# Kernel optimization log

Hardware: AMD Instinct MI355X
Metric: run time of the kernel (lower is better)

The kernel has to match this reference:

```python
import jax, jax.numpy as jnp
import numpy as np
from jax import lax

DIM = 256
NUM_HEADS = 8
HEAD_DIM = DIM // NUM_HEADS
SCALE = HEAD_DIM ** -0.5
DBZ_THRESHOLD = 15.0
DILATION = 1


def setup_inputs() -> dict:
    key = jax.random.key(0)
    k_x, k_dbz, k_qkv, k_pw, k_pb = jax.random.split(key, 5)
    B, T, H, W, C = 1, 4, 32, 32, DIM
    x = jax.random.normal(k_x, (B, T, H, W, C), dtype=jnp.float32)
    dbz_values = jax.random.uniform(k_dbz, (B, T, H, W, 1), dtype=jnp.float32) * 75.0
    s = 1.0 / np.sqrt(C)
    qkv_w = jax.random.uniform(k_qkv, (3 * C, C), minval=-s, maxval=s, dtype=jnp.float32)
    proj_w = jax.random.uniform(k_pw, (C, C), minval=-s, maxval=s, dtype=jnp.float32)
    proj_b = jax.random.uniform(k_pb, (C,), minval=-s, maxval=s, dtype=jnp.float32)
    return {"x": x, "dbz_values": dbz_values, "qkv_w": qkv_w, "proj_w": proj_w, "proj_b": proj_b}


def _keep_mask(dbz_values):
    # valid precipitation tokens
    valid = dbz_values[..., 0] >= DBZ_THRESHOLD  # (B,T,H,W) bool
    B, T, H, W = valid.shape
    ksz = 2 * DILATION + 1
    vf = valid.astype(jnp.float32).reshape(B * T, H, W)
    # morphological dilation == max-pool (stride 1, zero-pad). Padding with -inf is
    # equivalent here since every window contains >=1 real pixel (value >= 0).
    dilated = lax.reduce_window(vf, -jnp.inf, lax.max,
                                (1, ksz, ksz), (1, 1, 1),
                                [(0, 0), (DILATION, DILATION), (DILATION, DILATION)])
    boundary = ((dilated > 0.5) != (vf > 0.5)).reshape(B, T, H, W)
    return valid | boundary  # hybrid keep mask


def reference(x, dbz_values, qkv_w, proj_w, proj_b):
    B, T, H, W, C = x.shape
    keep = _keep_mask(dbz_values).reshape(-1)          # (N,) over all B*T*H*W tokens
    x_flat = x.reshape(-1, C)                          # (N,C)
    N = x_flat.shape[0]

    # QKV projection (no bias)
    qkv = (x_flat @ qkv_w.T).reshape(N, 3, NUM_HEADS, HEAD_DIM)
    q = jnp.transpose(qkv[:, 0], (1, 0, 2))           # (h,N,d)
    k = jnp.transpose(qkv[:, 1], (1, 0, 2))
    v = jnp.transpose(qkv[:, 2], (1, 0, 2))

    # dense attention among kept tokens == masked attention over all tokens:
    # mask non-kept KEYS with -inf; zero out non-kept QUERY outputs afterwards.
    attn = jnp.einsum('hnd,hmd->hnm', q, k) * SCALE    # (h,N,N)
    attn = jnp.where(keep[None, None, :], attn, -jnp.inf)
    attn = jax.nn.softmax(attn, axis=-1)
    out = jnp.einsum('hnm,hmd->hnd', attn, v)          # (h,N,d)
    out = jnp.transpose(out, (1, 0, 2)).reshape(N, C)
    out = out @ proj_w.T + proj_b
    out = jnp.where(keep[:, None], out, 0.0).reshape(B, T, H, W, C)
    return out + x  # residual
```

## Files before the change

### kernel.cpp

```cpp
#include <hip/hip_runtime.h>
#include <hip/hip_bf16.h>

#define N_TOK 4096
#define NH 8
#define HD 32
#define CDIM 256
#define QKV_N 768
#define VT_STRIDE 4128
#define XB_STRIDE 272
#define SCALE_F 0.17677669529663687f
#define LOG2E   1.4426950408889634f

typedef float  f32x4  __attribute__((ext_vector_type(4)));
typedef int    i32x4  __attribute__((ext_vector_type(4)));
typedef short  s16x4  __attribute__((ext_vector_type(4)));
typedef __bf16 bf16x8 __attribute__((ext_vector_type(8)));

union FragI { i32x4 i; bf16x8 b; };
union FragH { struct { s16x4 lo, hi; } s; bf16x8 b; };

__device__ inline int pack_bf16_trunc(float a, float b) {
  return (int)__builtin_amdgcn_perm(__builtin_bit_cast(unsigned, b),
                                    __builtin_bit_cast(unsigned, a),
                                    0x07060302u);
}

#define SEG_X 1048576
#define SEG_W (SEG_X + 196608)
#define SEG_P (SEG_W + 65536)
#define SEG_M (SEG_P + 4096)
__global__ __launch_bounds__(256) void fused_prep(const float* __restrict__ x,
                                                  const float* __restrict__ qkv_w,
                                                  const float* __restrict__ proj_w,
                                                  const float* __restrict__ dbz,
                                                  __bf16* __restrict__ xb,
                                                  __bf16* __restrict__ wqkvb,
                                                  __bf16* __restrict__ wprojb,
                                                  float* __restrict__ bias,
                                                  int* __restrict__ keepi) {
  int gid = blockIdx.x * 256 + threadIdx.x;
  if (gid < SEG_X) {
    xb[(gid >> 8) * XB_STRIDE + (gid & 255)] = (__bf16)x[gid];
  } else if (gid < SEG_W) {
    int i = gid - SEG_X;
    float s = ((i >> 8) < 256) ? (SCALE_F * LOG2E) : 1.0f;
    wqkvb[(i >> 8) * XB_STRIDE + (i & 255)] = (__bf16)(qkv_w[i] * s);
  } else if (gid < SEG_P) {
    int i = gid - SEG_W;
    wprojb[(i >> 8) * XB_STRIDE + (i & 255)] = (__bf16)proj_w[i];
  } else if (gid < SEG_M) {
    int n = gid - SEG_P;
    int t = n >> 10, rc = n & 1023, r = rc >> 5, c = rc & 31;
    bool keep = false;
    #pragma unroll
    for (int dr = -1; dr <= 1; dr++)
      #pragma unroll
      for (int dc = -1; dc <= 1; dc++) {
        int rr = r + dr, cc = c + dc;
        if (rr >= 0 && rr < 32 && cc >= 0 && cc < 32)
          keep = keep || (dbz[t * 1024 + rr * 32 + cc] >= 15.0f);
      }
    bias[n]  = keep ? 0.0f : -30000.0f;
    keepi[n] = keep ? 1 : 0;
  }
}

__global__ __launch_bounds__(256) void qkv_gemm(const __bf16* __restrict__ xb,
                                                const __bf16* __restrict__ wb,
                                                __bf16* __restrict__ qb,
                                                __bf16* __restrict__ kb,
                                                __bf16* __restrict__ vt) {
  int wave = threadIdx.x >> 6, lane = threadIdx.x & 63;
  int quad = lane >> 4, l16 = lane & 15;
  int m0 = blockIdx.x * 64 + wave * 16;
  int n0 = blockIdx.y * 64;

  const __bf16* xrow = xb + (size_t)(m0 + l16) * XB_STRIDE + quad * 8;
  const __bf16* wrow = wb + (size_t)(n0 + l16) * XB_STRIDE + quad * 8;

  FragI xc, wc[4];
  xc.i = *(const i32x4*)(xrow);
  #pragma unroll
  for (int nt = 0; nt < 4; nt++)
    wc[nt].i = *(const i32x4*)(wrow + (size_t)nt * 16 * XB_STRIDE);

  f32x4 acc[4] = {};
  for (int kk = 0; kk < CDIM; kk += 32) {
    int kn = (kk + 32 < CDIM) ? kk + 32 : 0;
    FragI xn, wn[4];
    xn.i = *(const i32x4*)(xrow + kn);
    #pragma unroll
    for (int nt = 0; nt < 4; nt++)
      wn[nt].i = *(const i32x4*)(wrow + (size_t)nt * 16 * XB_STRIDE + kn);
    #pragma unroll
    for (int nt = 0; nt < 4; nt++)
      acc[nt] = __builtin_amdgcn_mfma_f32_16x16x32_bf16(wc[nt].b, xc.b, acc[nt], 0, 0, 0);
    xc = xn;
    #pragma unroll
    for (int nt = 0; nt < 4; nt++) wc[nt] = wn[nt];
  }
  int m = m0 + l16;
  #pragma unroll
  for (int nt = 0; nt < 4; nt++) {
    int cbase = n0 + nt * 16 + quad * 4;
    int which = cbase >> 8, rem = cbase & 255, hd = rem >> 5, d0 = rem & 31;
    if (which < 2) {
      union { s16x4 s; __bf16 h[4]; } u;
      #pragma unroll
      for (int r = 0; r < 4; r++) u.h[r] = (__bf16)acc[nt][r];
      __bf16* dst = (which == 0 ? qb : kb) + ((size_t)hd * N_TOK + m) * HD + d0;
      *(s16x4*)dst = u.s;
    } else {
      #pragma unroll
      for (int r = 0; r < 4; r++)
        vt[(size_t)(hd * HD + d0 + r) * VT_STRIDE + m] = (__bf16)acc[nt][r];
    }
  }
}

__global__ __launch_bounds__(256, 2) void attn_kernel(const __bf16* __restrict__ qb,
                                                      const __bf16* __restrict__ kb,
                                                      const __bf16* __restrict__ vt,
                                                      const float* __restrict__ bias,
                                                      __bf16* __restrict__ ob) {
  __shared__ float red_o[4][64][34];
  __shared__ float red_l[4][64];

  int b = blockIdx.x;
  int head = b & 7, qx = b >> 3;
  int wave = threadIdx.x >> 6, lane = threadIdx.x & 63;
  int quad = lane >> 4, l16 = lane & 15;
  int q0 = qx * 64;

  const __bf16* qh = qb + (size_t)head * N_TOK * HD;
  const __bf16* kh = kb + (size_t)head * N_TOK * HD;
  const __bf16* vh = vt + (size_t)head * HD * VT_STRIDE;

  FragI qf[4];
  #pragma unroll
  for (int g = 0; g < 4; g++)
    qf[g].i = *(const i32x4*)(qh + (size_t)(q0 + g * 16 + l16) * HD + quad * 8);

  FragI ones;
  #pragma unroll
  for (int j = 0; j < 8; j++) ones.b[j] = (__bf16)1.0f;

  f32x4 o_lo[4] = {}, o_hi[4] = {}, lacc[4] = {};

  FragI ka_c, kb_c;
  f32x4 ba_c, bb_c;
  {
    int k0 = wave * 32;
    ka_c.i = *(const i32x4*)(kh + (size_t)(k0 + l16) * HD + quad * 8);
    kb_c.i = *(const i32x4*)(kh + (size_t)(k0 + 16 + l16) * HD + quad * 8);
    ba_c = *(const f32x4*)(bias + k0 + quad * 4);
    bb_c = *(const f32x4*)(bias + k0 + 16 + quad * 4);
  }

  for (int t = 0; t < 32; t++) {
    int kc = wave * 32 + t * 128;
    int kn = (t < 31) ? kc + 128 : wave * 32;

    FragI ka_n, kb_n;
    f32x4 ba_n, bb_n;
    ka_n.i = *(const i32x4*)(kh + (size_t)(kn + l16) * HD + quad * 8);
    kb_n.i = *(const i32x4*)(kh + (size_t)(kn + 16 + l16) * HD + quad * 8);
    ba_n = *(const f32x4*)(bias + kn + quad * 4);
    bb_n = *(const f32x4*)(bias + kn + 16 + quad * 4);

    FragH vlo, vhi;
    const __bf16* vp = vh + (size_t)l16 * VT_STRIDE + kc + quad * 4;
    vlo.s.lo = *(const s16x4*)(vp);
    vlo.s.hi = *(const s16x4*)(vp + 16);
    const __bf16* vp2 = vh + (size_t)(16 + l16) * VT_STRIDE + kc + quad * 4;
    vhi.s.lo = *(const s16x4*)(vp2);
    vhi.s.hi = *(const s16x4*)(vp2 + 16);

    f32x4 sa[4], sb[4];
    #pragma unroll
    for (int g = 0; g < 4; g++) {
      sa[g] = __builtin_amdgcn_mfma_f32_16x16x32_bf16(ka_c.b, qf[g].b, ba_c, 0, 0, 0);
      sb[g] = __builtin_amdgcn_mfma_f32_16x16x32_bf16(kb_c.b, qf[g].b, bb_c, 0, 0, 0);
    }

    FragI pf[4];
    #pragma unroll
    for (int g = 0; g < 4; g++) {
      float e0 = __builtin_amdgcn_exp2f(sa[g][0]);
      float e1 = __builtin_amdgcn_exp2f(sa[g][1]);
      float e2 = __builtin_amdgcn_exp2f(sa[g][2]);
      float e3 = __builtin_amdgcn_exp2f(sa[g][3]);
      float e4 = __builtin_amdgcn_exp2f(sb[g][0]);
      float e5 = __builtin_amdgcn_exp2f(sb[g][1]);
      float e6 = __builtin_amdgcn_exp2f(sb[g][2]);
      float e7 = __builtin_amdgcn_exp2f(sb[g][3]);
      pf[g].i[0] = pack_bf16_trunc(e0, e1);
      pf[g].i[1] = pack_bf16_trunc(e2, e3);
      pf[g].i[2] = pack_bf16_trunc(e4, e5);
      pf[g].i[3] = pack_bf16_trunc(e6, e7);
    }

    #pragma unroll
    for (int g = 0; g < 4; g++) {
      o_lo[g] = __builtin_amdgcn_mfma_f32_16x16x32_bf16(vlo.b, pf[g].b, o_lo[g], 0, 0, 0);
      o_hi[g] = __builtin_amdgcn_mfma_f32_16x16x32_bf16(vhi.b, pf[g].b, o_hi[g], 0, 0, 0);
      lacc[g] = __builtin_amdgcn_mfma_f32_16x16x32_bf16(ones.b, pf[g].b, lacc[g], 0, 0, 0);
    }

    ka_c = ka_n; kb_c = kb_n; ba_c = ba_n; bb_c = bb_n;
  }

  #pragma unroll
  for (int g = 0; g < 4; g++) {
    int q = g * 16 + l16;
    #pragma unroll
    for (int r = 0; r < 4; r++) {
      red_o[wave][q][quad * 4 + r]      = o_lo[g][r];
      red_o[wave][q][16 + quad * 4 + r] = o_hi[g][r];
    }
    if (quad == 0) red_l[wave][q] = lacc[g][0];
  }
  __syncthreads();

  int q = wave * 16 + l16;
  float lt = red_l[0][q] + red_l[1][q] + red_l[2][q] + red_l[3][q];
  float inv = 1.0f / lt;
  f32x4 slo = {0.f, 0.f, 0.f, 0.f}, shi = {0.f, 0.f, 0.f, 0.f};
  #pragma unroll
  for (int src = 0; src < 4; src++) {
    #pragma unroll
    for (int r = 0; r < 4; r++) {
      slo[r] += red_o[src][q][quad * 4 + r];
      shi[r] += red_o[src][q][16 + quad * 4 + r];
    }
  }
  union { s16x4 s; __bf16 h[4]; } u1, u2;
  #pragma unroll
  for (int r = 0; r < 4; r++) {
    u1.h[r] = (__bf16)(slo[r] * inv);
    u2.h[r] = (__bf16)(shi[r] * inv);
  }
  __bf16* orow = ob + (size_t)(q0 + q) * XB_STRIDE + head * HD;
  *(s16x4*)(orow + quad * 4)      = u1.s;
  *(s16x4*)(orow + 16 + quad * 4) = u2.s;
}

__global__ __launch_bounds__(256) void proj_gemm(const __bf16* __restrict__ ob,
                                                 const __bf16* __restrict__ wb,
                                                 const float* __restrict__ pb,
                                                 const int* __restrict__ keepi,
                                                 const float* __restrict__ x,
                                                 float* __restrict__ out) {
  int wave = threadIdx.x >> 6, lane = threadIdx.x & 63;
  int quad = lane >> 4, l16 = lane & 15;
  int m0 = blockIdx.x * 64 + wave * 16;
  int n0 = blockIdx.y * 64;

  const __bf16* arow = ob + (size_t)(m0 + l16) * XB_STRIDE + quad * 8;
  const __bf16* wrow = wb + (size_t)(n0 + l16) * XB_STRIDE + quad * 8;

  FragI ac, wc[4];
  ac.i = *(const i32x4*)(arow);
  #pragma unroll
  for (int nt = 0; nt < 4; nt++)
    wc[nt].i = *(const i32x4*)(wrow + (size_t)nt * 16 * XB_STRIDE);

  f32x4 acc[4] = {};
  for (int kk = 0; kk < CDIM; kk += 32) {
    int kn = (kk + 32 < CDIM) ? kk + 32 : 0;
    FragI an, wn[4];
    an.i = *(const i32x4*)(arow + kn);
    #pragma unroll
    for (int nt = 0; nt < 4; nt++)
      wn[nt].i = *(const i32x4*)(wrow + (size_t)nt * 16 * XB_STRIDE + kn);
    #pragma unroll
    for (int nt = 0; nt < 4; nt++)
      acc[nt] = __builtin_amdgcn_mfma_f32_16x16x32_bf16(wc[nt].b, ac.b, acc[nt], 0, 0, 0);
    ac = an;
    #pragma unroll
    for (int nt = 0; nt < 4; nt++) wc[nt] = wn[nt];
  }
  int m = m0 + l16;
  int keep = keepi[m];
  #pragma unroll
  for (int nt = 0; nt < 4; nt++) {
    int c0 = n0 + nt * 16 + quad * 4;
    #pragma unroll
    for (int r = 0; r < 4; r++) {
      float v = acc[nt][r] + pb[c0 + r];
      v = keep ? v : 0.0f;
      out[(size_t)m * CDIM + c0 + r] = v + x[(size_t)m * CDIM + c0 + r];
    }
  }
}

extern "C" void kernel_launch(void* const* d_in, const int* in_sizes, int n_in,
                              void* d_out, int out_size, void* d_ws, size_t ws_size,
                              hipStream_t stream) {
  const float* x      = (const float*)d_in[0];
  const float* dbz    = (const float*)d_in[1];
  const float* qkv_w  = (const float*)d_in[2];
  const float* proj_w = (const float*)d_in[3];
  const float* proj_b = (const float*)d_in[4];
  float* out = (float*)d_out;

  char* w = (char*)d_ws;
  __bf16* xb     = (__bf16*)(w);
  __bf16* qb     = (__bf16*)(w + (3u << 20));
  __bf16* kb     = (__bf16*)(w + (5u << 20));
  __bf16* vt     = (__bf16*)(w + (7u << 20));
  __bf16* ob     = (__bf16*)(w + (9u << 20) + (512u << 10));
  __bf16* wqkvb  = (__bf16*)(w + (12u << 20));
  __bf16* wprojb = (__bf16*)(w + (12u << 20) + (512u << 10));
  float*  bias   = (float*)(w + (13u << 20));
  int*    keepi  = (int*)(w + (13u << 20) + 16384);

  fused_prep<<<dim3(SEG_M / 256), dim3(256), 0, stream>>>(
      x, qkv_w, proj_w, dbz, xb, wqkvb, wprojb, bias, keepi);
  qkv_gemm<<<dim3(N_TOK / 64, QKV_N / 64), dim3(256), 0, stream>>>(
      xb, wqkvb, qb, kb, vt);
  attn_kernel<<<dim3((N_TOK / 64) * NH), dim3(256), 0, stream>>>(
      qb, kb, vt, bias, ob);
  proj_gemm<<<dim3(N_TOK / 64, CDIM / 64), dim3(256), 0, stream>>>(
      ob, wprojb, proj_b, keepi, x, out);
}
```

Measured before the change: 113.7 us.

## Permute V-transpose layout for single 128-bit loads and double-buffer V prefetch

The QKV kernel now writes the transposed V buffer with a permuted token order within each 32-token block. The attention kernel can then fetch each V fragment with one 16-byte load instead of two 8-byte loads. V loads are also prefetched one iteration ahead, alongside K and bias, using a two-slot register ring with unroll 4. This is meant to cut load instruction count and hide V latency, at the cost of extra register pressure under the 2-blocks-per-CU launch bound.

```diff
diff --git a/kernel.cpp b/kernel.cpp
--- a/kernel.cpp
+++ b/kernel.cpp
@@ -17,7 +17,6 @@
 typedef __bf16 bf16x8 __attribute__((ext_vector_type(8)));
 
 union FragI { i32x4 i; bf16x8 b; };
-union FragH { struct { s16x4 lo, hi; } s; bf16x8 b; };
 
 __device__ inline int pack_bf16_trunc(float a, float b) {
   return (int)__builtin_amdgcn_perm(__builtin_bit_cast(unsigned, b),
@@ -100,6 +99,7 @@
     for (int nt = 0; nt < 4; nt++) wc[nt] = wn[nt];
   }
   int m = m0 + l16;
+  int mperm = (m & ~31) + ((l16 >> 2) * 8) + (l16 & 3) + ((m & 16) ? 4 : 0);
   #pragma unroll
   for (int nt = 0; nt < 4; nt++) {
     int cbase = n0 + nt * 16 + quad * 4;
@@ -113,7 +113,7 @@
     } else {
       #pragma unroll
       for (int r = 0; r < 4; r++)
-        vt[(size_t)(hd * HD + d0 + r) * VT_STRIDE + m] = (__bf16)acc[nt][r];
+        vt[(size_t)(hd * HD + d0 + r) * VT_STRIDE + mperm] = (__bf16)acc[nt][r];
     }
   }
 }
@@ -147,40 +147,35 @@
 
   f32x4 o_lo[4] = {}, o_hi[4] = {}, lacc[4] = {};
 
-  FragI ka_c, kb_c;
-  f32x4 ba_c, bb_c;
+  FragI ka[2], kx[2], vlo[2], vhi[2];
+  f32x4 ba[2], bb[2];
   {
     int k0 = wave * 32;
-    ka_c.i = *(const i32x4*)(kh + (size_t)(k0 + l16) * HD + quad * 8);
-    kb_c.i = *(const i32x4*)(kh + (size_t)(k0 + 16 + l16) * HD + quad * 8);
-    ba_c = *(const f32x4*)(bias + k0 + quad * 4);
-    bb_c = *(const f32x4*)(bias + k0 + 16 + quad * 4);
-  }
-
+    ka[0].i  = *(const i32x4*)(kh + (size_t)(k0 + l16) * HD + quad * 8);
+    kx[0].i  = *(const i32x4*)(kh + (size_t)(k0 + 16 + l16) * HD + quad * 8);
+    ba[0] = *(const f32x4*)(bias + k0 + quad * 4);
+    bb[0] = *(const f32x4*)(bias + k0 + 16 + quad * 4);
+    vlo[0].i = *(const i32x4*)(vh + (size_t)l16 * VT_STRIDE + k0 + quad * 8);
+    vhi[0].i = *(const i32x4*)(vh + (size_t)(16 + l16) * VT_STRIDE + k0 + quad * 8);
+  }
+
+  #pragma unroll 4
   for (int t = 0; t < 32; t++) {
-    int kc = wave * 32 + t * 128;
-    int kn = (t < 31) ? kc + 128 : wave * 32;
-
-    FragI ka_n, kb_n;
-    f32x4 ba_n, bb_n;
-    ka_n.i = *(const i32x4*)(kh + (size_t)(kn + l16) * HD + quad * 8);
-    kb_n.i = *(const i32x4*)(kh + (size_t)(kn + 16 + l16) * HD + quad * 8);
-    ba_n = *(const f32x4*)(bias + kn + quad * 4);
-    bb_n = *(const f32x4*)(bias + kn + 16 + quad * 4);
-
-    FragH vlo, vhi;
-    const __bf16* vp = vh + (size_t)l16 * VT_STRIDE + kc + quad * 4;
-    vlo.s.lo = *(const s16x4*)(vp);
-    vlo.s.hi = *(const s16x4*)(vp + 16);
-    const __bf16* vp2 = vh + (size_t)(16 + l16) * VT_STRIDE + kc + quad * 4;
-    vhi.s.lo = *(const s16x4*)(vp2);
-    vhi.s.hi = *(const s16x4*)(vp2 + 16);
+    int cur = t & 1, nxt = cur ^ 1;
+    int kn = (t < 31) ? wave * 32 + (t + 1) * 128 : wave * 32;
+
+    ka[nxt].i  = *(const i32x4*)(kh + (size_t)(kn + l16) * HD + quad * 8);
+    kx[nxt].i  = *(const i32x4*)(kh + (size_t)(kn + 16 + l16) * HD + quad * 8);
+    ba[nxt] = *(const f32x4*)(bias + kn + quad * 4);
+    bb[nxt] = *(const f32x4*)(bias + kn + 16 + quad * 4);
+    vlo[nxt].i = *(const i32x4*)(vh + (size_t)l16 * VT_STRIDE + kn + quad * 8);
+    vhi[nxt].i = *(const i32x4*)(vh + (size_t)(16 + l16) * VT_STRIDE + kn + quad * 8);
 
     f32x4 sa[4], sb[4];
     #pragma unroll
     for (int g = 0; g < 4; g++) {
-      sa[g] = __builtin_amdgcn_mfma_f32_16x16x32_bf16(ka_c.b, qf[g].b, ba_c, 0, 0, 0);
-      sb[g] = __builtin_amdgcn_mfma_f32_16x16x32_bf16(kb_c.b, qf[g].b, bb_c, 0, 0, 0);
+      sa[g] = __builtin_amdgcn_mfma_f32_16x16x32_bf16(ka[cur].b, qf[g].b, ba[cur], 0, 0, 0);
+      sb[g] = __builtin_amdgcn_mfma_f32_16x16x32_bf16(kx[cur].b, qf[g].b, bb[cur], 0, 0, 0);
     }
 
     FragI pf[4];
@@ -202,12 +197,10 @@
 
     #pragma unroll
     for (int g = 0; g < 4; g++) {
-      o_lo[g] = __builtin_amdgcn_mfma_f32_16x16x32_bf16(vlo.b, pf[g].b, o_lo[g], 0, 0, 0);
-      o_hi[g] = __builtin_amdgcn_mfma_f32_16x16x32_bf16(vhi.b, pf[g].b, o_hi[g], 0, 0, 0);
+      o_lo[g] = __builtin_amdgcn_mfma_f32_16x16x32_bf16(vlo[cur].b, pf[g].b, o_lo[g], 0, 0, 0);
+      o_hi[g] = __builtin_amdgcn_mfma_f32_16x16x32_bf16(vhi[cur].b, pf[g].b, o_hi[g], 0, 0, 0);
       lacc[g] = __builtin_amdgcn_mfma_f32_16x16x32_bf16(ones.b, pf[g].b, lacc[g], 0, 0, 0);
     }
-
-    ka_c = ka_n; kb_c = kb_n; ba_c = ba_n; bb_c = bb_n;
   }
 
   #pragma unroll
```

Result: no change. 114.7 us (+0.9%).
